# Kernel optimization log

Measured on AMD Instinct MI355X. Metric: run time of the kernel, lower is better.

Reference implementation:

```python
import jax, jax.numpy as jnp
import numpy as np

IN_CH = 256
OUT_CH = 64
HEADS = 8


def setup_inputs() -> dict:
    key = jax.random.key(0)
    ks = jax.random.split(key, 7)
    N = 4096
    proj = OUT_CH * HEADS
    s_in = 1.0 / np.sqrt(IN_CH)
    return {
        "query_input": jax.random.normal(ks[0], (N, IN_CH), dtype=jnp.float32),
        "Wq": jax.random.uniform(ks[1], (proj, IN_CH), jnp.float32, -s_in, s_in),
        "bq": jax.random.uniform(ks[2], (proj,), jnp.float32, -s_in, s_in),
        "Wk": jax.random.uniform(ks[3], (proj, IN_CH), jnp.float32, -s_in, s_in),
        "bk": jax.random.uniform(ks[4], (proj,), jnp.float32, -s_in, s_in),
        "Wv": jax.random.uniform(ks[5], (proj, IN_CH), jnp.float32, -s_in, s_in),
        "bv": jax.random.uniform(ks[6], (proj,), jnp.float32, -s_in, s_in),
    }


def reference(query_input, Wq, bq, Wk, bk, Wv, bv):
    N = query_input.shape[0]
    # projections -> [N, H, M]
    q = (query_input @ Wq.T + bq).reshape(N, HEADS, OUT_CH)
    k = (query_input @ Wk.T + bk).reshape(N, HEADS, OUT_CH)
    v = (query_input @ Wv.T + bv).reshape(N, HEADS, OUT_CH)
    # sigmoid attention scores [N, L, H]
    attention_num = jax.nn.sigmoid(jnp.einsum('nhm,lhm->nlh', q, k))
    # sum-normalization over L (keys)
    normalizer = attention_num.sum(axis=1, keepdims=True)  # [N, 1, H]
    attention = attention_num / normalizer
    # weighted V reduction [N, H, D], then mean over heads -> [N, D]
    out = jnp.einsum('nlh,lhd->nhd', attention, v).mean(axis=1)
    return out
```

## Files before the change

kernel.cpp:

```cpp
#include <hip/hip_runtime.h>
#include <hip/hip_bf16.h>
#include <math.h>

#define N_TOK 4096
#define IN_CH 256
#define OUT_CH 64
#define HEADS 8
#define PROJ (OUT_CH * HEADS)
#define NLOG2E -1.44269504088896340736f

typedef float f32x4 __attribute__((ext_vector_type(4)));
typedef float f32x16 __attribute__((ext_vector_type(16)));
typedef __bf16 bf16x8 __attribute__((ext_vector_type(8)));
typedef unsigned short ushort_t;
typedef _Float16 f16_t;

__device__ inline ushort_t bf16rne(float x) {
    unsigned u = __float_as_uint(x);
    unsigned r = (u + 0x7FFFu + ((u >> 16) & 1u)) >> 16;
    return (ushort_t)r;
}

__device__ inline unsigned cvtpk_bf16(float lo, float hi) {
    unsigned d;
    asm("v_cvt_pk_bf16_f32 %0, %1, %2" : "=v"(d) : "v"(lo), "v"(hi));
    return d;
}
#define PLSWAP(x, y) asm("v_permlane32_swap_b32 %0, %1" : "+v"(x), "+v"(y))


__device__ inline void gld_lds16(const ushort_t* g, ushort_t* l) {
    __builtin_amdgcn_global_load_lds(
        (const __attribute__((address_space(1))) unsigned int*)g,
        (__attribute__((address_space(3))) unsigned int*)l,
        16, 0, 0);
}

__global__ __launch_bounds__(256) void cast_pack_kernel(
    const float* __restrict__ X,
    const float* __restrict__ Wq, const float* __restrict__ Wk,
    const float* __restrict__ Wv,
    ushort_t* __restrict__ Xa, ushort_t* __restrict__ Wp)
{
    const int i = blockIdx.x * 256 + threadIdx.x;
    const float* src;
    ushort_t* dst;
    float scale = 1.0f;
    if (i < 131072) {
        const int t = i & 15, quad = (i >> 4) & 3, k8 = (i >> 6) & 7, g = i >> 9;
        src = X + (size_t)(g * 16 + t) * IN_CH + k8 * 32 + quad * 8;
        dst = Xa + (size_t)i * 8;
    } else {
        const int j = i - 131072;
        const int z = j >> 14;
        const int r = j & 16383;
        const int cl = r & 15, quad = (r >> 4) & 3, k8 = (r >> 6) & 7, gc = r >> 9;
        const float* W = (z == 0) ? Wq : (z == 1) ? Wk : Wv;
        src = W + (size_t)(gc * 16 + cl) * IN_CH + k8 * 32 + quad * 8;
        dst = Wp + (size_t)z * 131072 * 8 + (size_t)r * 8;
        if (z == 0) scale = NLOG2E;
    }
    float4 a = *(const float4*)src;
    float4 b = *(const float4*)(src + 4);
    ushort_t pk[8];
    pk[0] = bf16rne(a.x * scale); pk[1] = bf16rne(a.y * scale);
    pk[2] = bf16rne(a.z * scale); pk[3] = bf16rne(a.w * scale);
    pk[4] = bf16rne(b.x * scale); pk[5] = bf16rne(b.y * scale);
    pk[6] = bf16rne(b.z * scale); pk[7] = bf16rne(b.w * scale);
    *(uint4*)dst = *(uint4*)pk;
}

__global__ __launch_bounds__(256) void proj_mfma_kernel(
    const ushort_t* __restrict__ Xa, const ushort_t* __restrict__ Wp,
    const float* __restrict__ bq, const float* __restrict__ bk,
    const float* __restrict__ bv,
    ushort_t* __restrict__ Qb, ushort_t* __restrict__ Kb,
    ushort_t* __restrict__ Vt)
{
    const int z = blockIdx.z;
    const float* bias = (z == 0) ? bq : (z == 1) ? bk : bv;
    const float bscale = (z == 0) ? NLOG2E : 1.0f;
    const int c0 = blockIdx.x * 64;
    const int n0 = blockIdx.y * 64;

    const int tid = threadIdx.x;
    const int w = tid >> 6;
    const int lane = tid & 63;
    const int l15 = lane & 15;
    const int quad = lane >> 4;

    __shared__ ushort_t Ws[2 * 2048];
    __shared__ ushort_t Es[64 * 68];

    const ushort_t* xa = Xa + (size_t)(blockIdx.y * 4 + w) * 4096 + lane * 8;
    const ushort_t* wsrc = Wp + (size_t)z * 131072 * 8 +
                           (size_t)(blockIdx.x * 4 + w) * 4096 + lane * 8;

    f32x4 acc[4] = {{0.f, 0.f, 0.f, 0.f}, {0.f, 0.f, 0.f, 0.f},
                    {0.f, 0.f, 0.f, 0.f}, {0.f, 0.f, 0.f, 0.f}};

    gld_lds16(wsrc, &Ws[w * 512]);

#pragma unroll
    for (int k8 = 0; k8 < 8; ++k8) {
        const int bo = (k8 & 1) * 2048;
        __syncthreads();
        if (k8 < 7)
            gld_lds16(wsrc + (k8 + 1) * 512,
                      &Ws[((k8 + 1) & 1) * 2048 + w * 512]);
        bf16x8 a = *(const bf16x8*)(xa + k8 * 512);
#pragma unroll
        for (int f = 0; f < 4; ++f) {
            bf16x8 b = *(const bf16x8*)&Ws[bo + f * 512 + lane * 8];
            acc[f] = __builtin_amdgcn_mfma_f32_16x16x32_bf16(a, b, acc[f], 0, 0, 0);
        }
    }

    if (z < 2) {
#pragma unroll
        for (int f = 0; f < 4; ++f) {
            const float bb = bias[c0 + f * 16 + l15] * bscale;
#pragma unroll
            for (int r = 0; r < 4; ++r)
                Es[(w * 16 + quad * 4 + r) * 68 + f * 16 + l15] = bf16rne(acc[f][r] + bb);
        }
    } else {
#pragma unroll
        for (int f = 0; f < 4; ++f) {
            const float bb = bias[c0 + f * 16 + l15];
#pragma unroll
            for (int r = 0; r < 4; ++r)
                Es[(f * 16 + l15) * 68 + w * 16 + quad * 4 + r] = bf16rne(acc[f][r] + bb);
        }
    }
    __syncthreads();

    const int erow = tid >> 2;
    const int ecol = (tid & 3) * 16;
    uint4 pk0 = *(uint4*)&Es[erow * 68 + ecol];
    uint4 pk1 = *(uint4*)&Es[erow * 68 + ecol + 8];
    if (z < 2) {
        ushort_t* out = z ? Kb : Qb;
        ushort_t* p = &out[(size_t)(n0 + erow) * PROJ + c0 + ecol];
        *(uint4*)p = pk0;
        *(uint4*)(p + 8) = pk1;
    } else {
        ushort_t* p = &Vt[(size_t)(c0 + erow) * N_TOK + n0 + ecol];
        *(uint4*)p = pk0;
        *(uint4*)(p + 8) = pk1;
    }
}

template<int ZS>
__global__ __launch_bounds__(256, 4) void attn_kernel(
    const ushort_t* __restrict__ Qb, const ushort_t* __restrict__ Kb,
    const ushort_t* __restrict__ Vt,
    f16_t* __restrict__ NUM, float* __restrict__ DEN)
{
    constexpr int KEYS = N_TOK / ZS;
    constexpr int TILES = KEYS / 64;

    const int h = blockIdx.y;
    const int z = blockIdx.z;
    const int n0 = blockIdx.x * 128;
    const int tid = threadIdx.x;
    const int w = tid >> 6;
    const int lane = tid & 63;
    const int l31 = lane & 31;
    const int hf = lane >> 5;

    __shared__ ushort_t Ks[2 * 64 * 64];
    __shared__ ushort_t Vs[2 * 64 * 64];

    bf16x8 qb[4];
    {
        const ushort_t* base = Qb + (size_t)(n0 + w * 32 + l31) * PROJ + h * 64 + hf * 8;
        qb[0] = *(const bf16x8*)(base);
        qb[1] = *(const bf16x8*)(base + 16);
        qb[2] = *(const bf16x8*)(base + 32);
        qb[3] = *(const bf16x8*)(base + 48);
    }

    bf16x8 onesv;
#pragma unroll
    for (int j = 0; j < 8; ++j) onesv[j] = (__bf16)1.0f;

    f32x16 o0 = {};
    f32x16 o1 = {};
    f32x16 dacc = {};

    const int lrow = lane >> 3;
    const int pc = lane & 7;
    const int swz = (pc ^ lrow) * 8;
    const int lb = w * 1024;
    const ushort_t* kg = Kb + (size_t)h * 64 +
                         ((size_t)z * KEYS + w * 16 + lrow) * PROJ + swz;
    const ushort_t* vg = Vt + ((size_t)h * 64 + w * 16 + lrow) * N_TOK +
                         (size_t)z * KEYS + swz;

    const int xm = l31 & 7;

    gld_lds16(kg,             &Ks[lb]);
    gld_lds16(kg + 8 * PROJ,  &Ks[lb + 512]);
    gld_lds16(vg,             &Vs[lb]);
    gld_lds16(vg + 8 * N_TOK, &Vs[lb + 512]);
    kg += 64 * PROJ;
    vg += 64;

    for (int lt = 0; lt < TILES; ++lt) {
        const int bo = (lt & 1) << 12;
        __syncthreads();
        if (lt + 1 < TILES) {
            const int bw = ((lt + 1) & 1) << 12;
            gld_lds16(kg,             &Ks[bw + lb]);
            gld_lds16(kg + 8 * PROJ,  &Ks[bw + lb + 512]);
            gld_lds16(vg,             &Vs[bw + lb]);
            gld_lds16(vg + 8 * N_TOK, &Vs[bw + lb + 512]);
            kg += 64 * PROJ;
            vg += 64;
        }

        {
            f32x16 s0 = {};
            __builtin_amdgcn_s_setprio(1);
#pragma unroll
            for (int ks = 0; ks < 4; ++ks) {
                const int pos = ((ks * 2 + hf) ^ xm) * 8;
                bf16x8 ka = *(const bf16x8*)&Ks[bo + l31 * 64 + pos];
                s0 = __builtin_amdgcn_mfma_f32_32x32x16_bf16(ka, qb[ks], s0, 0, 0, 0);
            }
            __builtin_amdgcn_s_setprio(0);

            float p[16];
#pragma unroll
            for (int r = 0; r < 16; ++r) {
                p[r] = __builtin_amdgcn_rcpf(1.0f + __builtin_amdgcn_exp2f(s0[r]));
            }
            unsigned d00 = cvtpk_bf16(p[0],  p[1]);
            unsigned d01 = cvtpk_bf16(p[2],  p[3]);
            unsigned d10 = cvtpk_bf16(p[4],  p[5]);
            unsigned d11 = cvtpk_bf16(p[6],  p[7]);
            unsigned d20 = cvtpk_bf16(p[8],  p[9]);
            unsigned d21 = cvtpk_bf16(p[10], p[11]);
            unsigned d30 = cvtpk_bf16(p[12], p[13]);
            unsigned d31 = cvtpk_bf16(p[14], p[15]);
            PLSWAP(d00, d10);
            PLSWAP(d01, d11);
            PLSWAP(d20, d30);
            PLSWAP(d21, d31);
            union { unsigned u[4]; bf16x8 v; } A0, A1;
            A0.u[0] = d00; A0.u[1] = d01; A0.u[2] = d10; A0.u[3] = d11;
            A1.u[0] = d20; A1.u[1] = d21; A1.u[2] = d30; A1.u[3] = d31;

            __builtin_amdgcn_s_setprio(1);
            {
                const int pos = ((0 + hf) ^ xm) * 8;
                bf16x8 vb0 = *(const bf16x8*)&Vs[bo + l31 * 64 + pos];
                o0 = __builtin_amdgcn_mfma_f32_32x32x16_bf16(A0.v, vb0, o0, 0, 0, 0);
                bf16x8 vb1 = *(const bf16x8*)&Vs[bo + (32 + l31) * 64 + pos];
                o1 = __builtin_amdgcn_mfma_f32_32x32x16_bf16(A0.v, vb1, o1, 0, 0, 0);
            }
            dacc = __builtin_amdgcn_mfma_f32_32x32x16_bf16(A0.v, onesv, dacc, 0, 0, 0);
            {
                const int pos = ((2 + hf) ^ xm) * 8;
                bf16x8 vb0 = *(const bf16x8*)&Vs[bo + l31 * 64 + pos];
                o0 = __builtin_amdgcn_mfma_f32_32x32x16_bf16(A1.v, vb0, o0, 0, 0, 0);
                bf16x8 vb1 = *(const bf16x8*)&Vs[bo + (32 + l31) * 64 + pos];
                o1 = __builtin_amdgcn_mfma_f32_32x32x16_bf16(A1.v, vb1, o1, 0, 0, 0);
            }
            dacc = __builtin_amdgcn_mfma_f32_32x32x16_bf16(A1.v, onesv, dacc, 0, 0, 0);
            __builtin_amdgcn_s_setprio(0);
        }

        {
            f32x16 s1 = {};
            __builtin_amdgcn_s_setprio(1);
#pragma unroll
            for (int ks = 0; ks < 4; ++ks) {
                const int pos = ((ks * 2 + hf) ^ xm) * 8;
                bf16x8 ka = *(const bf16x8*)&Ks[bo + (32 + l31) * 64 + pos];
                s1 = __builtin_amdgcn_mfma_f32_32x32x16_bf16(ka, qb[ks], s1, 0, 0, 0);
            }
            __builtin_amdgcn_s_setprio(0);

            float p[16];
#pragma unroll
            for (int r = 0; r < 16; ++r) {
                p[r] = __builtin_amdgcn_rcpf(1.0f + __builtin_amdgcn_exp2f(s1[r]));
            }
            unsigned e00 = cvtpk_bf16(p[0],  p[1]);
            unsigned e01 = cvtpk_bf16(p[2],  p[3]);
            unsigned e10 = cvtpk_bf16(p[4],  p[5]);
            unsigned e11 = cvtpk_bf16(p[6],  p[7]);
            unsigned e20 = cvtpk_bf16(p[8],  p[9]);
            unsigned e21 = cvtpk_bf16(p[10], p[11]);
            unsigned e30 = cvtpk_bf16(p[12], p[13]);
            unsigned e31 = cvtpk_bf16(p[14], p[15]);
            PLSWAP(e00, e10);
            PLSWAP(e01, e11);
            PLSWAP(e20, e30);
            PLSWAP(e21, e31);
            union { unsigned u[4]; bf16x8 v; } A2, A3;
            A2.u[0] = e00; A2.u[1] = e01; A2.u[2] = e10; A2.u[3] = e11;
            A3.u[0] = e20; A3.u[1] = e21; A3.u[2] = e30; A3.u[3] = e31;

            __builtin_amdgcn_s_setprio(1);
            {
                const int pos = ((4 + hf) ^ xm) * 8;
                bf16x8 vb0 = *(const bf16x8*)&Vs[bo + l31 * 64 + pos];
                o0 = __builtin_amdgcn_mfma_f32_32x32x16_bf16(A2.v, vb0, o0, 0, 0, 0);
                bf16x8 vb1 = *(const bf16x8*)&Vs[bo + (32 + l31) * 64 + pos];
                o1 = __builtin_amdgcn_mfma_f32_32x32x16_bf16(A2.v, vb1, o1, 0, 0, 0);
            }
            dacc = __builtin_amdgcn_mfma_f32_32x32x16_bf16(A2.v, onesv, dacc, 0, 0, 0);
            {
                const int pos = ((6 + hf) ^ xm) * 8;
                bf16x8 vb0 = *(const bf16x8*)&Vs[bo + l31 * 64 + pos];
                o0 = __builtin_amdgcn_mfma_f32_32x32x16_bf16(A3.v, vb0, o0, 0, 0, 0);
                bf16x8 vb1 = *(const bf16x8*)&Vs[bo + (32 + l31) * 64 + pos];
                o1 = __builtin_amdgcn_mfma_f32_32x32x16_bf16(A3.v, vb1, o1, 0, 0, 0);
            }
            dacc = __builtin_amdgcn_mfma_f32_32x32x16_bf16(A3.v, onesv, dacc, 0, 0, 0);
            __builtin_amdgcn_s_setprio(0);
        }
    }

#pragma unroll
    for (int rq = 0; rq < 4; ++rq) {
#pragma unroll
        for (int j = 0; j < 4; ++j) {
            const int q = n0 + w * 32 + rq * 8 + hf * 4 + j;
            f16_t* np_ = &NUM[((size_t)z * N_TOK + q) * PROJ + h * 64 + l31];
            np_[0]  = (f16_t)o0[rq * 4 + j];
            np_[32] = (f16_t)o1[rq * 4 + j];
        }
    }
    if (l31 == 0) {
#pragma unroll
        for (int r = 0; r < 16; ++r) {
            const int q = n0 + w * 32 + (r & 3) + 8 * (r >> 2) + 4 * hf;
            DEN[((size_t)z * N_TOK + q) * HEADS + h] = dacc[r];
        }
    }
}

template<int ZS>
__global__ __launch_bounds__(256) void reduce_kernel(
    const f16_t* __restrict__ NUM, const float* __restrict__ DEN,
    float* __restrict__ out)
{
    const int g = blockIdx.x * 256 + threadIdx.x;
    const int n = g >> 6;
    const int d = g & 63;
    float acc = 0.0f;
#pragma unroll
    for (int hh = 0; hh < HEADS; ++hh) {
        float num = 0.0f, dd = 0.0f;
#pragma unroll
        for (int zz = 0; zz < ZS; ++zz) {
            num += (float)NUM[((size_t)zz * N_TOK + n) * PROJ + hh * 64 + d];
            dd  += DEN[((size_t)zz * N_TOK + n) * HEADS + hh];
        }
        acc += num / dd;
    }
    out[g] = acc * 0.125f;
}

extern "C" void kernel_launch(void* const* d_in, const int* in_sizes, int n_in,
                              void* d_out, int out_size, void* d_ws, size_t ws_size,
                              hipStream_t stream) {
    (void)in_sizes; (void)n_in; (void)out_size;
    const float* X  = (const float*)d_in[0];
    const float* Wq = (const float*)d_in[1];
    const float* bq = (const float*)d_in[2];
    const float* Wk = (const float*)d_in[3];
    const float* bk = (const float*)d_in[4];
    const float* Wv = (const float*)d_in[5];
    const float* bv = (const float*)d_in[6];
    float* out = (float*)d_out;

    const size_t NEED4 =
        (size_t)4 * N_TOK * PROJ * 2 + (size_t)4 * N_TOK * HEADS * 4 +
        (size_t)3 * N_TOK * PROJ * 2 + (size_t)N_TOK * IN_CH * 2 +
        (size_t)3 * PROJ * IN_CH * 2;
    const int ZS = (ws_size >= NEED4) ? 4 : 2;

    f16_t* NUM = (f16_t*)d_ws;
    float* DEN = (float*)(NUM + (size_t)ZS * N_TOK * PROJ);
    ushort_t* Qb = (ushort_t*)(DEN + (size_t)ZS * N_TOK * HEADS);
    ushort_t* Kb = Qb + (size_t)N_TOK * PROJ;
    ushort_t* Vt = Kb + (size_t)N_TOK * PROJ;
    ushort_t* Xa = Vt + (size_t)N_TOK * PROJ;
    ushort_t* Wp = Xa + (size_t)N_TOK * IN_CH;

    cast_pack_kernel<<<dim3(704), 256, 0, stream>>>(X, Wq, Wk, Wv, Xa, Wp);
    proj_mfma_kernel<<<dim3(PROJ / 64, N_TOK / 64, 3), 256, 0, stream>>>(
        Xa, Wp, bq, bk, bv, Qb, Kb, Vt);
    if (ZS == 4) {
        attn_kernel<4><<<dim3(N_TOK / 128, HEADS, 4), 256, 0, stream>>>(
            Qb, Kb, Vt, NUM, DEN);
        reduce_kernel<4><<<dim3(N_TOK * OUT_CH / 256), 256, 0, stream>>>(
            NUM, DEN, out);
    } else {
        attn_kernel<2><<<dim3(N_TOK / 128, HEADS, 2), 256, 0, stream>>>(
            Qb, Kb, Vt, NUM, DEN);
        reduce_kernel<2><<<dim3(N_TOK * OUT_CH / 256), 256, 0, stream>>>(
            NUM, DEN, out);
    }
}
```

Before: 128.8 us.

## Fuse fp32-to-bf16 cast/pack into projection kernel, drop separate cast pass

Removes the standalone cast_pack kernel and instead has the projection kernel read fp32 X and W directly, converting to bf16 in registers. The weight tile for all K steps is staged in LDS once, which replaces the double-buffered async LDS loads, and X fragments are converted per lane on the fly. This saves one kernel launch and the round trip through the packed workspace buffers. In exchange, each block re-reads and re-converts fp32 data: X is read once per column block and per Q/K/V, so global traffic and ALU work for conversion grow.

```diff
diff --git a/kernel.cpp b/kernel.cpp
--- a/kernel.cpp
+++ b/kernel.cpp
@@ -36,49 +36,19 @@
         16, 0, 0);
 }
 
-__global__ __launch_bounds__(256) void cast_pack_kernel(
+__global__ __launch_bounds__(256) void proj_mfma_kernel(
     const float* __restrict__ X,
     const float* __restrict__ Wq, const float* __restrict__ Wk,
     const float* __restrict__ Wv,
-    ushort_t* __restrict__ Xa, ushort_t* __restrict__ Wp)
-{
-    const int i = blockIdx.x * 256 + threadIdx.x;
-    const float* src;
-    ushort_t* dst;
-    float scale = 1.0f;
-    if (i < 131072) {
-        const int t = i & 15, quad = (i >> 4) & 3, k8 = (i >> 6) & 7, g = i >> 9;
-        src = X + (size_t)(g * 16 + t) * IN_CH + k8 * 32 + quad * 8;
-        dst = Xa + (size_t)i * 8;
-    } else {
-        const int j = i - 131072;
-        const int z = j >> 14;
-        const int r = j & 16383;
-        const int cl = r & 15, quad = (r >> 4) & 3, k8 = (r >> 6) & 7, gc = r >> 9;
-        const float* W = (z == 0) ? Wq : (z == 1) ? Wk : Wv;
-        src = W + (size_t)(gc * 16 + cl) * IN_CH + k8 * 32 + quad * 8;
-        dst = Wp + (size_t)z * 131072 * 8 + (size_t)r * 8;
-        if (z == 0) scale = NLOG2E;
-    }
-    float4 a = *(const float4*)src;
-    float4 b = *(const float4*)(src + 4);
-    ushort_t pk[8];
-    pk[0] = bf16rne(a.x * scale); pk[1] = bf16rne(a.y * scale);
-    pk[2] = bf16rne(a.z * scale); pk[3] = bf16rne(a.w * scale);
-    pk[4] = bf16rne(b.x * scale); pk[5] = bf16rne(b.y * scale);
-    pk[6] = bf16rne(b.z * scale); pk[7] = bf16rne(b.w * scale);
-    *(uint4*)dst = *(uint4*)pk;
-}
-
-__global__ __launch_bounds__(256) void proj_mfma_kernel(
-    const ushort_t* __restrict__ Xa, const ushort_t* __restrict__ Wp,
     const float* __restrict__ bq, const float* __restrict__ bk,
     const float* __restrict__ bv,
     ushort_t* __restrict__ Qb, ushort_t* __restrict__ Kb,
     ushort_t* __restrict__ Vt)
 {
     const int z = blockIdx.z;
+    const float* W    = (z == 0) ? Wq : (z == 1) ? Wk : Wv;
     const float* bias = (z == 0) ? bq : (z == 1) ? bk : bv;
+    const float wscale = (z == 0) ? NLOG2E : 1.0f;
     const float bscale = (z == 0) ? NLOG2E : 1.0f;
     const int c0 = blockIdx.x * 64;
     const int n0 = blockIdx.y * 64;
@@ -89,32 +59,45 @@
     const int l15 = lane & 15;
     const int quad = lane >> 4;
 
-    __shared__ ushort_t Ws[2 * 2048];
-    __shared__ ushort_t Es[64 * 68];
-
-    const ushort_t* xa = Xa + (size_t)(blockIdx.y * 4 + w) * 4096 + lane * 8;
-    const ushort_t* wsrc = Wp + (size_t)z * 131072 * 8 +
-                           (size_t)(blockIdx.x * 4 + w) * 4096 + lane * 8;
+    __shared__ ushort_t Ws[8 * 2048];
+    ushort_t* Es = Ws;
+
+    {
+        const float* wsrc = W + (size_t)(c0 + w * 16 + l15) * IN_CH + quad * 8;
+#pragma unroll
+        for (int k8 = 0; k8 < 8; ++k8) {
+            float4 a = *(const float4*)(wsrc + k8 * 32);
+            float4 b = *(const float4*)(wsrc + k8 * 32 + 4);
+            ushort_t pk[8];
+            pk[0] = bf16rne(a.x * wscale); pk[1] = bf16rne(a.y * wscale);
+            pk[2] = bf16rne(a.z * wscale); pk[3] = bf16rne(a.w * wscale);
+            pk[4] = bf16rne(b.x * wscale); pk[5] = bf16rne(b.y * wscale);
+            pk[6] = bf16rne(b.z * wscale); pk[7] = bf16rne(b.w * wscale);
+            *(uint4*)&Ws[k8 * 2048 + w * 512 + lane * 8] = *(uint4*)pk;
+        }
+    }
+    __syncthreads();
 
     f32x4 acc[4] = {{0.f, 0.f, 0.f, 0.f}, {0.f, 0.f, 0.f, 0.f},
                     {0.f, 0.f, 0.f, 0.f}, {0.f, 0.f, 0.f, 0.f}};
 
-    gld_lds16(wsrc, &Ws[w * 512]);
-
+    const float* xsrc = X + (size_t)(n0 + w * 16 + l15) * IN_CH + quad * 8;
 #pragma unroll
     for (int k8 = 0; k8 < 8; ++k8) {
-        const int bo = (k8 & 1) * 2048;
-        __syncthreads();
-        if (k8 < 7)
-            gld_lds16(wsrc + (k8 + 1) * 512,
-                      &Ws[((k8 + 1) & 1) * 2048 + w * 512]);
-        bf16x8 a = *(const bf16x8*)(xa + k8 * 512);
+        float4 xa = *(const float4*)(xsrc + k8 * 32);
+        float4 xb = *(const float4*)(xsrc + k8 * 32 + 4);
+        union { ushort_t u[8]; bf16x8 v; } ax;
+        ax.u[0] = bf16rne(xa.x); ax.u[1] = bf16rne(xa.y);
+        ax.u[2] = bf16rne(xa.z); ax.u[3] = bf16rne(xa.w);
+        ax.u[4] = bf16rne(xb.x); ax.u[5] = bf16rne(xb.y);
+        ax.u[6] = bf16rne(xb.z); ax.u[7] = bf16rne(xb.w);
 #pragma unroll
         for (int f = 0; f < 4; ++f) {
-            bf16x8 b = *(const bf16x8*)&Ws[bo + f * 512 + lane * 8];
-            acc[f] = __builtin_amdgcn_mfma_f32_16x16x32_bf16(a, b, acc[f], 0, 0, 0);
-        }
-    }
+            bf16x8 b = *(const bf16x8*)&Ws[k8 * 2048 + f * 512 + lane * 8];
+            acc[f] = __builtin_amdgcn_mfma_f32_16x16x32_bf16(ax.v, b, acc[f], 0, 0, 0);
+        }
+    }
+    __syncthreads();
 
     if (z < 2) {
 #pragma unroll
@@ -381,8 +364,7 @@
 
     const size_t NEED4 =
         (size_t)4 * N_TOK * PROJ * 2 + (size_t)4 * N_TOK * HEADS * 4 +
-        (size_t)3 * N_TOK * PROJ * 2 + (size_t)N_TOK * IN_CH * 2 +
-        (size_t)3 * PROJ * IN_CH * 2;
+        (size_t)3 * N_TOK * PROJ * 2;
     const int ZS = (ws_size >= NEED4) ? 4 : 2;
 
     f16_t* NUM = (f16_t*)d_ws;
@@ -390,12 +372,9 @@
     ushort_t* Qb = (ushort_t*)(DEN + (size_t)ZS * N_TOK * HEADS);
     ushort_t* Kb = Qb + (size_t)N_TOK * PROJ;
     ushort_t* Vt = Kb + (size_t)N_TOK * PROJ;
-    ushort_t* Xa = Vt + (size_t)N_TOK * PROJ;
-    ushort_t* Wp = Xa + (size_t)N_TOK * IN_CH;
-
-    cast_pack_kernel<<<dim3(704), 256, 0, stream>>>(X, Wq, Wk, Wv, Xa, Wp);
+
     proj_mfma_kernel<<<dim3(PROJ / 64, N_TOK / 64, 3), 256, 0, stream>>>(
-        Xa, Wp, bq, bk, bv, Qb, Kb, Vt);
+        X, Wq, Wk, Wv, bq, bk, bv, Qb, Kb, Vt);
     if (ZS == 4) {
         attn_kernel<4><<<dim3(N_TOK / 128, HEADS, 4), 256, 0, stream>>>(
             Qb, Kb, Vt, NUM, DEN);
```

Measured after the change: 144.0 us. 1.12x slower.
